# Kernel optimization log

Hardware: AMD Instinct MI355X
Metric: run time of the kernel (lower is better)

## Reference

```python
import jax, jax.numpy as jnp
import numpy as np

EMBED = 512
HEADS = 8
HEAD_DIM = EMBED // HEADS


def setup_inputs() -> dict:
    key = jax.random.key(0)
    ks = jax.random.split(key, 7)
    N, Q, K = 8, 2048, 4096
    s = 1.0 / np.sqrt(EMBED)
    return {
        "x": jax.random.normal(ks[0], (N, Q, EMBED), dtype=jnp.float32),
        "y": jax.random.normal(ks[1], (N, K, EMBED), dtype=jnp.float32),
        "Wq": jax.random.normal(ks[2], (EMBED, EMBED), dtype=jnp.float32) * s,
        "Wk": jax.random.normal(ks[3], (EMBED, EMBED), dtype=jnp.float32) * s,
        "Wv": jax.random.normal(ks[4], (EMBED, EMBED), dtype=jnp.float32) * s,
        "Wo": jax.random.normal(ks[5], (EMBED, EMBED), dtype=jnp.float32) * s,
        "bo": jax.random.normal(ks[6], (EMBED,), dtype=jnp.float32) * 0.01,
    }


def reference(x, y, Wq, Wk, Wv, Wo, bo):
    N, Q, _ = x.shape
    K = y.shape[1]
    # torch Linear: out = in @ W.T
    queries = (x @ Wq.T).reshape(N, Q, HEADS, HEAD_DIM)
    keys = (y @ Wk.T).reshape(N, K, HEADS, HEAD_DIM)
    values = (y @ Wv.T).reshape(N, K, HEADS, HEAD_DIM)
    # NOTE: heads are SUMMED in the score einsum (head-collapsed attention)
    energy = jnp.einsum("nqhd,nkhd->nqk", queries, keys)  # [N,Q,K]
    attention = jax.nn.softmax(energy / jnp.sqrt(jnp.float32(EMBED)), axis=2)
    out = jnp.einsum("nqk,nkhd->nqhd", attention, values).reshape(N, Q, EMBED)
    return x + out @ Wo.T + bo
```

## Files before the change

### kernel.cpp

```cpp
#include <hip/hip_runtime.h>
#include <stdint.h>

typedef unsigned short u16;
typedef short bf16x8 __attribute__((ext_vector_type(8)));
typedef float f32x4 __attribute__((ext_vector_type(4)));
typedef u16 u16x8 __attribute__((ext_vector_type(8)));
typedef u16 u16x4v __attribute__((ext_vector_type(4)));
typedef uint32_t u32x4 __attribute__((ext_vector_type(4)));

#define EMBED 512
#define NBATCH 8
#define QLEN 2048
#define KLEN 4096

__device__ __forceinline__ u16 f2bf(float f) {
  uint32_t u = __builtin_bit_cast(uint32_t, f);
  u += 0x7fffu + ((u >> 16) & 1u);
  return (u16)(u >> 16);
}
__device__ __forceinline__ float bf2f(u16 b) {
  return __builtin_bit_cast(float, (uint32_t)b << 16);
}

__device__ __forceinline__ void gload_lds16(const void* g, void* lds) {
  __builtin_amdgcn_global_load_lds(
      (__attribute__((address_space(1))) void*)(uintptr_t)g,
      (__attribute__((address_space(3))) void*)(uint32_t)(uintptr_t)lds,
      16, 0, 0);
}

__global__ __launch_bounds__(256) void cvt_all_kernel(
    const float* __restrict__ x, const float* __restrict__ y,
    const float* __restrict__ wq, const float* __restrict__ wk,
    const float* __restrict__ wv, const float* __restrict__ wo,
    u16* __restrict__ dst) {
  const int64_t B0 = 2097152;
  const int64_t B1 = B0 + 4194304;
  const int64_t B2 = B1 + 65536;
  const int64_t B3 = B2 + 65536;
  const int64_t B4 = B3 + 65536;
  int64_t i = (int64_t)blockIdx.x * 256 + threadIdx.x;
  const float* src; int64_t off;
  if (i < B0)      { src = x;  off = 0;  }
  else if (i < B1) { src = y;  off = B0; }
  else if (i < B2) { src = wq; off = B1; }
  else if (i < B3) { src = wk; off = B2; }
  else if (i < B4) { src = wv; off = B3; }
  else             { src = wo; off = B4; }
  float4 f = ((const float4*)src)[i - off];
  u16x4v o = { f2bf(f.x), f2bf(f.y), f2bf(f.z), f2bf(f.w) };
  ((u16x4v*)dst)[i] = o;
}

constexpr int EPI_BF16 = 0;
constexpr int EPI_BF16_SCALE = 1;
constexpr int EPI_BF16_TRANS = 2;
constexpr int EPI_F32_RESID = 3;

template <int MODE>
__global__ __launch_bounds__(256, 2) void gemm_bt(
    const u16* __restrict__ A, const u16* __restrict__ B, void* __restrict__ Cv,
    int M, int N, int K,
    int64_t aBatch, int64_t bBatch, int64_t cBatch,
    float scale, const float* __restrict__ xres, const float* __restrict__ bias,
    u16* __restrict__ Vt) {
  __shared__ __align__(16) u16 As[128 * 64];
  __shared__ __align__(16) u16 Bs[128 * 64];

  const int tid = threadIdx.x;
  const int wave = tid >> 6;
  const int lane = tid & 63;
  const int bz = blockIdx.z;
  const int row0 = blockIdx.x * 128;
  const int col0 = blockIdx.y * 128;
  const u16* Ab = A + (int64_t)bz * aBatch;
  const u16* Bb = B + (int64_t)bz * bBatch;

  const int srow = wave * 32 + (lane >> 3);
  const int scol = (lane & 7) * 8;
  const u16* aSrc = Ab + (int64_t)(row0 + srow) * K + scol;
  const u16* bSrc = Bb + (int64_t)(col0 + srow) * K + scol;

  const int wm = (wave >> 1) * 64;
  const int wn = (wave & 1) * 64;
  const int fr = lane & 15;
  const int fq = lane >> 4;

  f32x4 acc[4][4];
#pragma unroll
  for (int mi = 0; mi < 4; ++mi)
#pragma unroll
    for (int ni = 0; ni < 4; ++ni) acc[mi][ni] = 0.0f;

  const int nkt = K >> 6;
  for (int kt = 0; kt < nkt; ++kt) {
    __syncthreads();
    const u16* aS = aSrc + kt * 64;
    const u16* bS = bSrc + kt * 64;
#pragma unroll
    for (int i = 0; i < 4; ++i) {
      gload_lds16(aS + (int64_t)(i * 8) * K, &As[(wave * 32 + i * 8) * 64]);
      gload_lds16(bS + (int64_t)(i * 8) * K, &Bs[(wave * 32 + i * 8) * 64]);
    }
    __syncthreads();
#pragma unroll
    for (int ks = 0; ks < 2; ++ks) {
      bf16x8 af[4], bfr[4];
#pragma unroll
      for (int mi = 0; mi < 4; ++mi)
        af[mi] = *(const bf16x8*)&As[(wm + mi * 16 + fr) * 64 + ks * 32 + fq * 8];
#pragma unroll
      for (int ni = 0; ni < 4; ++ni)
        bfr[ni] = *(const bf16x8*)&Bs[(wn + ni * 16 + fr) * 64 + ks * 32 + fq * 8];
#pragma unroll
      for (int mi = 0; mi < 4; ++mi)
#pragma unroll
        for (int ni = 0; ni < 4; ++ni)
          acc[mi][ni] = __builtin_amdgcn_mfma_f32_16x16x32_bf16(af[mi], bfr[ni],
                                                                acc[mi][ni], 0, 0, 0);
    }
  }

  if constexpr (MODE == EPI_BF16 || MODE == EPI_BF16_SCALE) {
    u16* C = (u16*)Cv + (int64_t)bz * cBatch;
#pragma unroll
    for (int mi = 0; mi < 4; ++mi) {
      const int rowb = row0 + wm + mi * 16 + fq * 4;
#pragma unroll
      for (int ni = 0; ni < 4; ++ni) {
        const int col = col0 + wn + ni * 16 + fr;
#pragma unroll
        for (int r = 0; r < 4; ++r) {
          float v = acc[mi][ni][r];
          if constexpr (MODE == EPI_BF16_SCALE) v *= scale;
          C[(int64_t)(rowb + r) * N + col] = f2bf(v);
        }
      }
    }
  } else if constexpr (MODE == EPI_BF16_TRANS) {
#pragma unroll
    for (int mi = 0; mi < 4; ++mi) {
      const int rowb = row0 + wm + mi * 16 + fq * 4;
      const int nb = rowb >> 12;
      const int kk = rowb & 4095;
#pragma unroll
      for (int ni = 0; ni < 4; ++ni) {
        const int col = col0 + wn + ni * 16 + fr;
        u16x4v o = { f2bf(acc[mi][ni][0]), f2bf(acc[mi][ni][1]),
                     f2bf(acc[mi][ni][2]), f2bf(acc[mi][ni][3]) };
        *(u16x4v*)&Vt[((int64_t)nb * EMBED + col) * KLEN + kk] = o;
      }
    }
  } else {
    float* C = (float*)Cv;
#pragma unroll
    for (int mi = 0; mi < 4; ++mi) {
      const int rowb = row0 + wm + mi * 16 + fq * 4;
#pragma unroll
      for (int ni = 0; ni < 4; ++ni) {
        const int col = col0 + wn + ni * 16 + fr;
        const float bv = bias[col];
#pragma unroll
        for (int r = 0; r < 4; ++r) {
          const int64_t idx = (int64_t)(rowb + r) * N + col;
          C[idx] = acc[mi][ni][r] + xres[idx] + bv;
        }
      }
    }
  }
}

__global__ __launch_bounds__(256, 1) void attn_kernel(
    const u16* __restrict__ Qm, const u16* __restrict__ Km,
    const u16* __restrict__ Vt, u16* __restrict__ O) {
  __shared__ __align__(16) u16 Ks[2][32 * 512];
  __shared__ __align__(16) u16 Vs[2][512 * 32];

  const int tid = threadIdx.x;
  const int w = tid >> 6;
  const int lane = tid & 63;
  const int fr = lane & 15, fq = lane >> 4;
  const int s7 = fr & 7;
  const int nb = blockIdx.x & 7;
  const int qt = blockIdx.x >> 3;

  bf16x8 q[16];
  {
    const u16* Qb = Qm + ((int64_t)nb * QLEN + qt * 64 + w * 16 + fr) * EMBED + fq * 8;
#pragma unroll
    for (int kc = 0; kc < 16; ++kc) q[kc] = *(const bf16x8*)&Qb[kc * 32];
  }

  f32x4 o[32];
#pragma unroll
  for (int i = 0; i < 32; ++i) o[i] = 0.0f;
  float mrun = -1e30f, lrun = 0.0f;

  const u16* Kb = Km + (int64_t)nb * KLEN * EMBED;
  const u16* Vb = Vt + (int64_t)nb * (int64_t)EMBED * KLEN;

  const int vrow = lane >> 2;
  const int vcl = (lane & 3) ^ (vrow & 3);

  {
    const u16* srcK = Kb + (int64_t)(w * 8) * EMBED;
#pragma unroll
    for (int i = 0; i < 8; ++i)
      gload_lds16(srcK + (int64_t)i * EMBED + (lane ^ i) * 8, &Ks[0][(w * 8 + i) * 512]);
#pragma unroll
    for (int i = 0; i < 8; ++i) {
      const int row0 = w * 128 + i * 16;
      gload_lds16(Vb + (int64_t)(row0 + vrow) * KLEN + vcl * 8, &Vs[0][row0 * 32]);
    }
  }
  __syncthreads();

  const int NT = KLEN / 32;
  for (int t = 0; t < NT; ++t) {
    const int cur = t & 1;
    if (t + 1 < NT) {
      const u16* srcK = Kb + ((int64_t)(t + 1) * 32 + w * 8) * EMBED;
#pragma unroll
      for (int i = 0; i < 8; ++i)
        gload_lds16(srcK + (int64_t)i * EMBED + (lane ^ i) * 8,
                    &Ks[cur ^ 1][(w * 8 + i) * 512]);
#pragma unroll
      for (int i = 0; i < 8; ++i) {
        const int row0 = w * 128 + i * 16;
        gload_lds16(Vb + (int64_t)(row0 + vrow) * KLEN + (t + 1) * 32 + vcl * 8,
                    &Vs[cur ^ 1][row0 * 32]);
      }
    }

    const u16* Kc = Ks[cur];
    f32x4 s0 = 0.0f, s1 = 0.0f;
#pragma unroll
    for (int kc = 0; kc < 16; ++kc) {
      bf16x8 k0 = *(const bf16x8*)&Kc[(fr)*512 + (((kc * 4 + fq) ^ s7) * 8)];
      bf16x8 k1 = *(const bf16x8*)&Kc[(16 + fr) * 512 + (((kc * 4 + fq) ^ s7) * 8)];
      s0 = __builtin_amdgcn_mfma_f32_16x16x32_bf16(k0, q[kc], s0, 0, 0, 0);
      s1 = __builtin_amdgcn_mfma_f32_16x16x32_bf16(k1, q[kc], s1, 0, 0, 0);
    }

    float mt = fmaxf(fmaxf(fmaxf(s0[0], s0[1]), fmaxf(s0[2], s0[3])),
                     fmaxf(fmaxf(s1[0], s1[1]), fmaxf(s1[2], s1[3])));
    mt = fmaxf(mt, __shfl_xor(mt, 16));
    mt = fmaxf(mt, __shfl_xor(mt, 32));
    float alpha = 1.0f;
    if (!__all(mt <= mrun + 8.0f)) {
      const float mn = fmaxf(mrun, mt);
      alpha = __expf(mrun - mn);
      lrun *= alpha;
      mrun = mn;
    }
    float p0[4], p1[4];
    float rs = 0.0f;
#pragma unroll
    for (int r = 0; r < 4; ++r) {
      p0[r] = __expf(s0[r] - mrun);
      p1[r] = __expf(s1[r] - mrun);
      rs += p0[r] + p1[r];
    }
    rs += __shfl_xor(rs, 16);
    rs += __shfl_xor(rs, 32);
    lrun += rs;

    const uint32_t lo0 = (uint32_t)f2bf(p0[0]) | ((uint32_t)f2bf(p0[1]) << 16);
    const uint32_t lo1 = (uint32_t)f2bf(p0[2]) | ((uint32_t)f2bf(p0[3]) << 16);
    const uint32_t hi0 = (uint32_t)f2bf(p1[0]) | ((uint32_t)f2bf(p1[1]) << 16);
    const uint32_t hi1 = (uint32_t)f2bf(p1[2]) | ((uint32_t)f2bf(p1[3]) << 16);
    const int srcA = fr + (((fq << 1) & 3) << 4);
    const int srcB = srcA + 16;
    const bool useHi = (fq >= 2);
    const uint32_t aLo0 = __shfl(lo0, srcA), aHi0 = __shfl(hi0, srcA);
    const uint32_t aLo1 = __shfl(lo1, srcA), aHi1 = __shfl(hi1, srcA);
    const uint32_t bLo0 = __shfl(lo0, srcB), bHi0 = __shfl(hi0, srcB);
    const uint32_t bLo1 = __shfl(lo1, srcB), bHi1 = __shfl(hi1, srcB);
    u32x4 pd;
    pd[0] = useHi ? aHi0 : aLo0;
    pd[1] = useHi ? aHi1 : aLo1;
    pd[2] = useHi ? bHi0 : bLo0;
    pd[3] = useHi ? bHi1 : bLo1;
    const bf16x8 pb = __builtin_bit_cast(bf16x8, pd);

    if (__any(alpha != 1.0f)) {
      float ra[4];
#pragma unroll
      for (int r = 0; r < 4; ++r) ra[r] = __shfl(alpha, (fq << 2) + r);
#pragma unroll
      for (int dt = 0; dt < 32; ++dt)
#pragma unroll
        for (int r = 0; r < 4; ++r) o[dt][r] *= ra[r];
    }

    const u16* Vc = Vs[cur];
#pragma unroll
    for (int dt = 0; dt < 32; ++dt) {
      bf16x8 vb = *(const bf16x8*)&Vc[(dt * 16 + fr) * 32 + ((fq ^ (fr & 3)) * 8)];
      o[dt] = __builtin_amdgcn_mfma_f32_16x16x32_bf16(pb, vb, o[dt], 0, 0, 0);
    }

    __syncthreads();
  }

  float linv[4];
#pragma unroll
  for (int r = 0; r < 4; ++r) linv[r] = 1.0f / __shfl(lrun, (fq << 2) + r);
  u16* Ob = O + ((int64_t)nb * QLEN + qt * 64 + w * 16) * EMBED;
#pragma unroll
  for (int dt = 0; dt < 32; ++dt)
#pragma unroll
    for (int r = 0; r < 4; ++r)
      Ob[(int64_t)((fq << 2) + r) * EMBED + dt * 16 + fr] = f2bf(o[dt][r] * linv[r]);
}

extern "C" void kernel_launch(void* const* d_in, const int* in_sizes, int n_in,
                              void* d_out, int out_size, void* d_ws, size_t ws_size,
                              hipStream_t stream) {
  const float* x  = (const float*)d_in[0];
  const float* y  = (const float*)d_in[1];
  const float* Wq = (const float*)d_in[2];
  const float* Wk = (const float*)d_in[3];
  const float* Wv = (const float*)d_in[4];
  const float* Wo = (const float*)d_in[5];
  const float* bo = (const float*)d_in[6];
  float* out = (float*)d_out;

  const int64_t nx = (int64_t)NBATCH * QLEN * EMBED;
  const int64_t ny = (int64_t)NBATCH * KLEN * EMBED;
  const int64_t nw = (int64_t)EMBED * EMBED;

  u16* w   = (u16*)d_ws;
  u16* xb  = w;
  u16* O   = w; w += nx;
  u16* yb  = w; w += ny;
  u16* Wqb = w; w += nw;
  u16* Wkb = w; w += nw;
  u16* Wvb = w; w += nw;
  u16* Wob = w; w += nw;
  u16* Qm  = w; w += nx;
  u16* Km  = w; w += ny;
  u16* Vt  = w; w += ny;

  cvt_all_kernel<<<25600, 256, 0, stream>>>(x, y, Wq, Wk, Wv, Wo, xb);

  const float scal = 0.04419417382415922f;
  gemm_bt<EPI_BF16_SCALE><<<dim3(128, 4, 1), 256, 0, stream>>>(
      xb, Wqb, Qm, 16384, EMBED, EMBED, 0, 0, 0, scal, nullptr, nullptr, nullptr);
  gemm_bt<EPI_BF16><<<dim3(256, 4, 1), 256, 0, stream>>>(
      yb, Wkb, Km, 32768, EMBED, EMBED, 0, 0, 0, 1.f, nullptr, nullptr, nullptr);
  gemm_bt<EPI_BF16_TRANS><<<dim3(256, 4, 1), 256, 0, stream>>>(
      yb, Wvb, nullptr, 32768, EMBED, EMBED, 0, 0, 0, 1.f, nullptr, nullptr, Vt);

  attn_kernel<<<NBATCH * 32, 256, 0, stream>>>(Qm, Km, Vt, O);

  gemm_bt<EPI_F32_RESID><<<dim3(128, 4, 1), 256, 0, stream>>>(
      O, Wob, out, 16384, EMBED, EMBED, 0, 0, 0, 1.f, x, bo, nullptr);
}
```

Before: 415.5 us.

## Repartition PV matmul so each wave owns a d-slice across all query rows

The P·V stage changes from each wave computing all 512 output columns for its own 16 queries to each wave computing 128 output columns for all 64 queries. P tiles and per-row rescale factors are exchanged through LDS with an added barrier, which replaces the cross-lane shuffles. Each wave now reads only its 128-row slice of the V tile into registers, cutting LDS reads of V by a factor of four, and the V swizzle pattern is changed to match. The cost is an extra block-wide barrier and LDS round-trip per key tile, plus a rescale check that now covers all 64 rows.

```diff
diff --git a/kernel.cpp b/kernel.cpp
--- a/kernel.cpp
+++ b/kernel.cpp
@@ -6,7 +6,7 @@
 typedef float f32x4 __attribute__((ext_vector_type(4)));
 typedef u16 u16x8 __attribute__((ext_vector_type(8)));
 typedef u16 u16x4v __attribute__((ext_vector_type(4)));
-typedef uint32_t u32x4 __attribute__((ext_vector_type(4)));
+typedef uint32_t u32x2 __attribute__((ext_vector_type(2)));
 
 #define EMBED 512
 #define NBATCH 8
@@ -175,12 +175,15 @@
     const u16* __restrict__ Vt, u16* __restrict__ O) {
   __shared__ __align__(16) u16 Ks[2][32 * 512];
   __shared__ __align__(16) u16 Vs[2][512 * 32];
+  __shared__ __align__(16) u16 Pls[4 * 512];
+  __shared__ __align__(16) float Als[64];
 
   const int tid = threadIdx.x;
   const int w = tid >> 6;
   const int lane = tid & 63;
   const int fr = lane & 15, fq = lane >> 4;
   const int s7 = fr & 7;
+  const int frk = fr & 6;
   const int nb = blockIdx.x & 7;
   const int qt = blockIdx.x >> 3;
 
@@ -200,7 +203,8 @@
   const u16* Vb = Vt + (int64_t)nb * (int64_t)EMBED * KLEN;
 
   const int vrow = lane >> 2;
-  const int vcl = (lane & 3) ^ (vrow & 3);
+  const int vcl = (lane & 3) ^ ((lane >> 3) & 3);
+  const int vswz = ((fr >> 1) & 3);
 
   {
     const u16* srcK = Kb + (int64_t)(w * 8) * EMBED;
@@ -241,6 +245,12 @@
       s0 = __builtin_amdgcn_mfma_f32_16x16x32_bf16(k0, q[kc], s0, 0, 0, 0);
       s1 = __builtin_amdgcn_mfma_f32_16x16x32_bf16(k1, q[kc], s1, 0, 0, 0);
     }
+
+    const u16* Vc = Vs[cur];
+    bf16x8 vb[8];
+#pragma unroll
+    for (int dt = 0; dt < 8; ++dt)
+      vb[dt] = *(const bf16x8*)&Vc[((w * 128 + dt * 16) + fr) * 32 + ((fq ^ vswz) * 8)];
 
     float mt = fmaxf(fmaxf(fmaxf(s0[0], s0[1]), fmaxf(s0[2], s0[3])),
                      fmaxf(fmaxf(s1[0], s1[1]), fmaxf(s1[2], s1[3])));
@@ -269,49 +279,68 @@
     const uint32_t lo1 = (uint32_t)f2bf(p0[2]) | ((uint32_t)f2bf(p0[3]) << 16);
     const uint32_t hi0 = (uint32_t)f2bf(p1[0]) | ((uint32_t)f2bf(p1[1]) << 16);
     const uint32_t hi1 = (uint32_t)f2bf(p1[2]) | ((uint32_t)f2bf(p1[3]) << 16);
-    const int srcA = fr + (((fq << 1) & 3) << 4);
-    const int srcB = srcA + 16;
-    const bool useHi = (fq >= 2);
-    const uint32_t aLo0 = __shfl(lo0, srcA), aHi0 = __shfl(hi0, srcA);
-    const uint32_t aLo1 = __shfl(lo1, srcA), aHi1 = __shfl(hi1, srcA);
-    const uint32_t bLo0 = __shfl(lo0, srcB), bHi0 = __shfl(hi0, srcB);
-    const uint32_t bLo1 = __shfl(lo1, srcB), bHi1 = __shfl(hi1, srcB);
-    u32x4 pd;
-    pd[0] = useHi ? aHi0 : aLo0;
-    pd[1] = useHi ? aHi1 : aLo1;
-    pd[2] = useHi ? bHi0 : bLo0;
-    pd[3] = useHi ? bHi1 : bLo1;
-    const bf16x8 pb = __builtin_bit_cast(bf16x8, pd);
-
-    if (__any(alpha != 1.0f)) {
-      float ra[4];
-#pragma unroll
-      for (int r = 0; r < 4; ++r) ra[r] = __shfl(alpha, (fq << 2) + r);
-#pragma unroll
-      for (int dt = 0; dt < 32; ++dt)
-#pragma unroll
-        for (int r = 0; r < 4; ++r) o[dt][r] *= ra[r];
-    }
-
-    const u16* Vc = Vs[cur];
-#pragma unroll
-    for (int dt = 0; dt < 32; ++dt) {
-      bf16x8 vb = *(const bf16x8*)&Vc[(dt * 16 + fr) * 32 + ((fq ^ (fr & 3)) * 8)];
-      o[dt] = __builtin_amdgcn_mfma_f32_16x16x32_bf16(pb, vb, o[dt], 0, 0, 0);
-    }
+    {
+      u32x2 wlo = {lo0, lo1}, whi = {hi0, hi1};
+      *(u32x2*)&Pls[w * 512 + fr * 32 + ((fq ^ frk) * 4)] = wlo;
+      *(u32x2*)&Pls[w * 512 + fr * 32 + (((4 + fq) ^ frk) * 4)] = whi;
+    }
+    if (fq == 0) Als[w * 16 + fr] = alpha;
+
+    asm volatile("s_waitcnt lgkmcnt(0)" ::: "memory");
+    __builtin_amdgcn_sched_barrier(0);
+    __builtin_amdgcn_s_barrier();
+    __builtin_amdgcn_sched_barrier(0);
+
+    f32x4 ra[4];
+#pragma unroll
+    for (int qg = 0; qg < 4; ++qg) ra[qg] = *(const f32x4*)&Als[qg * 16 + fq * 4];
+    int nz = 0;
+#pragma unroll
+    for (int qg = 0; qg < 4; ++qg)
+#pragma unroll
+      for (int r = 0; r < 4; ++r) nz |= (ra[qg][r] != 1.0f);
+    if (nz) {
+#pragma unroll
+      for (int qg = 0; qg < 4; ++qg)
+#pragma unroll
+        for (int dt = 0; dt < 8; ++dt)
+#pragma unroll
+          for (int r = 0; r < 4; ++r) o[qg * 8 + dt][r] *= ra[qg][r];
+    }
+
+    bf16x8 pa[4];
+#pragma unroll
+    for (int qg = 0; qg < 4; ++qg)
+      pa[qg] = *(const bf16x8*)&Pls[qg * 512 + fr * 32 + (((2 * fq) ^ frk) * 4)];
+
+#pragma unroll
+    for (int qg = 0; qg < 4; ++qg)
+#pragma unroll
+      for (int dt = 0; dt < 8; ++dt)
+        o[qg * 8 + dt] = __builtin_amdgcn_mfma_f32_16x16x32_bf16(pa[qg], vb[dt],
+                                                                 o[qg * 8 + dt], 0, 0, 0);
 
     __syncthreads();
   }
 
-  float linv[4];
-#pragma unroll
-  for (int r = 0; r < 4; ++r) linv[r] = 1.0f / __shfl(lrun, (fq << 2) + r);
-  u16* Ob = O + ((int64_t)nb * QLEN + qt * 64 + w * 16) * EMBED;
-#pragma unroll
-  for (int dt = 0; dt < 32; ++dt)
-#pragma unroll
-    for (int r = 0; r < 4; ++r)
-      Ob[(int64_t)((fq << 2) + r) * EMBED + dt * 16 + fr] = f2bf(o[dt][r] * linv[r]);
+  if (fq == 0) Als[w * 16 + fr] = lrun;
+  __syncthreads();
+  f32x4 li[4];
+#pragma unroll
+  for (int qg = 0; qg < 4; ++qg) {
+    f32x4 lv = *(const f32x4*)&Als[qg * 16 + fq * 4];
+#pragma unroll
+    for (int r = 0; r < 4; ++r) li[qg][r] = 1.0f / lv[r];
+  }
+  u16* Ob = O + ((int64_t)nb * QLEN + qt * 64) * EMBED + w * 128;
+#pragma unroll
+  for (int qg = 0; qg < 4; ++qg)
+#pragma unroll
+    for (int dt = 0; dt < 8; ++dt)
+#pragma unroll
+      for (int r = 0; r < 4; ++r)
+        Ob[(int64_t)(qg * 16 + fq * 4 + r) * EMBED + dt * 16 + fr] =
+            f2bf(o[qg * 8 + dt][r] * li[qg][r]);
 }
 
 extern "C" void kernel_launch(void* const* d_in, const int* in_sizes, int n_in,
```

Result: no change. 421.5 us (+1.4%).
